# Performance work log

Hardware: AMD Instinct MI355X
Metric: run time of the kernel (lower is better)

Reference implementation:

```python
import jax, jax.numpy as jnp
import numpy as np

N = 50000      # total nodes
E = 800000     # total edges (before self-loops)
B = 512        # graphs in batch
H = 4          # attention heads
D = 64         # per-head dim (hidden 256 = H*D)
F_IN = 203     # node feature dim
HID = H * D
NEG_SLOPE = 0.2  # PyG GATConv LeakyReLU default
LN_EPS = 1e-5


def setup_inputs() -> dict:
    key = jax.random.key(0)
    ks = jax.random.split(key, 24)
    g = lambda k, shape, fan: (jax.random.normal(k, shape, jnp.float32) / np.sqrt(fan))
    inp = {
        "x": jax.random.normal(ks[0], (N, F_IN), jnp.float32),
        "edge_index": jax.random.randint(ks[1], (2, E), 0, N, jnp.int64),
        "edge_weight": jax.random.uniform(ks[2], (E,), jnp.float32),
        "batch": jnp.sort(jax.random.randint(ks[3], (N,), 0, B, jnp.int64)),
        # GAT layer 1 params
        "W1": g(ks[4], (HID, F_IN), F_IN),
        "a_s1": g(ks[5], (H, D), D),
        "a_d1": g(ks[6], (H, D), D),
        "a_e1": g(ks[7], (H, D), D),
        "We1": g(ks[8], (HID, 1), 1),
        "b1": jnp.zeros((HID,), jnp.float32),
        # GAT layer 2 params
        "W2": g(ks[9], (HID, HID), HID),
        "a_s2": g(ks[10], (H, D), D),
        "a_d2": g(ks[11], (H, D), D),
        "a_e2": g(ks[12], (H, D), D),
        "We2": g(ks[13], (HID, 1), 1),
        "b2": jnp.zeros((HID,), jnp.float32),
        # LayerNorms
        "ln1_g": jnp.ones((HID,), jnp.float32),
        "ln1_b": jnp.zeros((HID,), jnp.float32),
        "ln2_g": jnp.ones((HID,), jnp.float32),
        "ln2_b": jnp.zeros((HID,), jnp.float32),
    }
    return inp


def _gat(x, src, dst, e_attr, W, a_s, a_d, a_e, We, bias, n_nodes):
    # projected node features: [N, H, D]
    xp = (x @ W.T).reshape(n_nodes, H, D)
    alpha_src = jnp.einsum('nhd,hd->nh', xp, a_s)   # [N, H]
    alpha_dst = jnp.einsum('nhd,hd->nh', xp, a_d)   # [N, H]
    ep = (e_attr @ We.T).reshape(-1, H, D)          # [E', H, D]
    alpha_edge = jnp.einsum('ehd,hd->eh', ep, a_e)  # [E', H]
    logits = jax.nn.leaky_relu(alpha_src[src] + alpha_dst[dst] + alpha_edge, NEG_SLOPE)
    # segment softmax over incoming edges per destination node
    m = jax.ops.segment_max(logits, dst, num_segments=n_nodes)
    ex = jnp.exp(logits - m[dst])
    denom = jax.ops.segment_sum(ex, dst, num_segments=n_nodes)
    alpha = ex / denom[dst]                          # [E', H]
    msg = alpha[:, :, None] * xp[src]                # [E', H, D]
    out = jax.ops.segment_sum(msg, dst, num_segments=n_nodes)
    return out.reshape(n_nodes, HID) + bias


def _ln(x, g, b):
    mu = x.mean(-1, keepdims=True)
    var = ((x - mu) ** 2).mean(-1, keepdims=True)
    return (x - mu) * jax.lax.rsqrt(var + LN_EPS) * g + b


def reference(x, edge_index, edge_weight, batch,
              W1, a_s1, a_d1, a_e1, We1, b1,
              W2, a_s2, a_d2, a_e2, We2, b2,
              ln1_g, ln1_b, ln2_g, ln2_b):
    n = x.shape[0]
    # PyG GATConv add_self_loops=True, edge_attr fill_value='mean'
    loop = jnp.arange(n)
    src = jnp.concatenate([edge_index[0], loop])
    dst = jnp.concatenate([edge_index[1], loop])
    ew = jnp.concatenate([edge_weight, jnp.full((n,), edge_weight.mean(), edge_weight.dtype)])
    e_attr = ew[:, None]  # edge_dim = 1

    h = _gat(x, src, dst, e_attr, W1, a_s1, a_d1, a_e1, We1, b1, n)
    h = jax.nn.elu(_ln(h, ln1_g, ln1_b))  # dropout omitted (eval mode)
    h = _gat(h, src, dst, e_attr, W2, a_s2, a_d2, a_e2, We2, b2, n)
    h = jax.nn.elu(_ln(h, ln2_g, ln2_b))

    # global_mean_pool
    s = jax.ops.segment_sum(h, batch, num_segments=B)
    cnt = jax.ops.segment_sum(jnp.ones((n,), h.dtype), batch, num_segments=B)
    return s / jnp.maximum(cnt, 1.0)[:, None]
```

## Files before the change

### kernel.cpp

```cpp
#include <hip/hip_runtime.h>
#include <math.h>

#define HID 256
#define NEG_SLOPE 0.2f
#define LN_EPS 1e-5f

typedef __attribute__((ext_vector_type(4))) float f32x4;
typedef __attribute__((ext_vector_type(8))) short bf16x8;
typedef __attribute__((address_space(3))) unsigned char lds_b;
typedef const __attribute__((address_space(1))) unsigned char glob_b;

__device__ __forceinline__ float bf2f_lo(unsigned int u) {
    union { unsigned int i; float f; } c; c.i = u << 16; return c.f;
}
__device__ __forceinline__ float bf2f_hi(unsigned int u) {
    union { unsigned int i; float f; } c; c.i = u & 0xffff0000u; return c.f;
}
__device__ __forceinline__ float bf2f_u(unsigned short u) {
    union { unsigned int i; float f; } c; c.i = ((unsigned int)u) << 16; return c.f;
}
__device__ __forceinline__ unsigned short f2bf(float f) {
    union { float f; unsigned int i; } c; c.f = f;
    unsigned int i = c.i;
    return (unsigned short)((i + 0x7fffu + ((i >> 16) & 1u)) >> 16);
}

__global__ __launch_bounds__(256) void k_pre(const float* __restrict__ ew, int E,
                                             const int* __restrict__ ei, int N, int EN, int NH,
                                             float* __restrict__ partials, int* __restrict__ deg,
                                             const float* __restrict__ W1, const float* __restrict__ W2,
                                             unsigned short* __restrict__ o1, unsigned short* __restrict__ o2, int K1,
                                             const float* __restrict__ x, unsigned short* __restrict__ x16, int FIN) {
    int t = threadIdx.x;
    int b = blockIdx.x;
    if (b < 256) {
        __shared__ float sdata[4];
        float v = 0.f;
        for (int i = b * 256 + t; i < E; i += 65536) v += ew[i];
        for (int o = 32; o; o >>= 1) v += __shfl_xor(v, o);
        if ((t & 63) == 0) sdata[t >> 6] = v;
        __syncthreads();
        if (t == 0) partials[b] = sdata[0] + sdata[1] + sdata[2] + sdata[3];
    } else if (b < 256 + NH) {
        int i = (b - 256) * 1024 + t;
        int e0 = i, e1 = i + 256, e2 = i + 512, e3 = i + 768;
        bool v0 = e0 < EN, v1 = e1 < EN, v2 = e2 < EN, v3 = e3 < EN;
        int d0 = v0 ? ((e0 < E) ? ei[E + e0] : e0 - E) : 0;
        int d1 = v1 ? ((e1 < E) ? ei[E + e1] : e1 - E) : 0;
        int d2 = v2 ? ((e2 < E) ? ei[E + e2] : e2 - E) : 0;
        int d3 = v3 ? ((e3 < E) ? ei[E + e3] : e3 - E) : 0;
        if (v0) atomicAdd(&deg[d0], 1);
        if (v1) atomicAdd(&deg[d1], 1);
        if (v2) atomicAdd(&deg[d2], 1);
        if (v3) atomicAdd(&deg[d3], 1);
    } else if (b < 256 + NH + 512) {
        int wb = b - 256 - NH;
        const float* in = (wb < 256) ? W1 : W2;
        unsigned short* out = (wb < 256) ? o1 : o2;
        int K = (wb < 256) ? K1 : 256;
        int col = wb & 255;
        float v = (t < K) ? in[(size_t)col * K + t] : 0.f;
        int ks = t >> 5, j = (t >> 3) & 3, e = t & 7;
        out[ks * 8192 + j * 2048 + ((((col << 4) ^ (j << 4))) >> 1) + e] = f2bf(v);
    } else {
        int r = b - 256 - NH - 512;
        x16[(size_t)r * 256 + t] = (t < FIN) ? f2bf(x[(size_t)r * FIN + t]) : (unsigned short)0;
    }
}

__global__ __launch_bounds__(256) void k_scanred_coeff(const int* __restrict__ deg, int N, int NB,
                                                       int* __restrict__ bsum,
                                                       const float* __restrict__ partials, float* __restrict__ sumw,
                                                       const float* __restrict__ We1, const float* __restrict__ ae1,
                                                       const float* __restrict__ We2, const float* __restrict__ ae2,
                                                       float* __restrict__ c1, float* __restrict__ c2) {
    int t = threadIdx.x;
    int b = blockIdx.x;
    if (b < NB) {
        __shared__ int sdata[4];
        int i = b * 256 + t;
        int v = (i < N) ? deg[i] : 0;
        for (int o = 32; o; o >>= 1) v += __shfl_xor(v, o);
        if ((t & 63) == 0) sdata[t >> 6] = v;
        __syncthreads();
        if (t == 0) bsum[b] = sdata[0] + sdata[1] + sdata[2] + sdata[3];
    } else if (b == NB) {
        __shared__ float sdata[4];
        float v = partials[t];
        for (int o = 32; o; o >>= 1) v += __shfl_xor(v, o);
        if ((t & 63) == 0) sdata[t >> 6] = v;
        __syncthreads();
        if (t == 0) *sumw = sdata[0] + sdata[1] + sdata[2] + sdata[3];
    } else {
        float v1 = We1[t] * ae1[t];
        float v2 = We2[t] * ae2[t];
        for (int o = 1; o < 64; o <<= 1) { v1 += __shfl_xor(v1, o); v2 += __shfl_xor(v2, o); }
        if ((t & 63) == 0) { c1[t >> 6] = v1; c2[t >> 6] = v2; }
    }
}

__global__ __launch_bounds__(256) void k_scan_apply(const int* __restrict__ deg, int N, int NB,
                                                    const int* __restrict__ bsum,
                                                    int* __restrict__ offs, int* __restrict__ cursor) {
    __shared__ int sm[256];
    __shared__ int sb[256];
    int t = threadIdx.x;
    int i = blockIdx.x * 256 + t;
    int v = (i < N) ? deg[i] : 0;
    int vb = (t < NB) ? bsum[t] : 0;
    sm[t] = v;
    sb[t] = vb;
    __syncthreads();
    for (int o = 1; o < 256; o <<= 1) {
        int tv = (t >= o) ? sm[t - o] : 0;
        int tb = (t >= o) ? sb[t - o] : 0;
        __syncthreads();
        sm[t] += tv;
        sb[t] += tb;
        __syncthreads();
    }
    int myb = bsum[blockIdx.x];
    int boff = sb[blockIdx.x] - myb;
    if (i < N) {
        int e = boff + sm[t] - v;
        offs[i] = e; cursor[i] = e;
        if (i == N - 1) offs[N] = boff + sm[t];
    }
}

__global__ __launch_bounds__(256) void k_scatter(const int* __restrict__ ei, int E, int EN,
                                                 int* __restrict__ cursor, int* __restrict__ csr_eid) {
    int i = blockIdx.x * 1024 + threadIdx.x;
    int e0 = i, e1 = i + 256, e2 = i + 512, e3 = i + 768;
    bool v0 = e0 < EN, v1 = e1 < EN, v2 = e2 < EN, v3 = e3 < EN;
    int d0 = v0 ? ((e0 < E) ? ei[E + e0] : e0 - E) : 0;
    int d1 = v1 ? ((e1 < E) ? ei[E + e1] : e1 - E) : 0;
    int d2 = v2 ? ((e2 < E) ? ei[E + e2] : e2 - E) : 0;
    int d3 = v3 ? ((e3 < E) ? ei[E + e3] : e3 - E) : 0;
    int p0 = v0 ? atomicAdd(&cursor[d0], 1) : 0;
    int p1 = v1 ? atomicAdd(&cursor[d1], 1) : 0;
    int p2 = v2 ? atomicAdd(&cursor[d2], 1) : 0;
    int p3 = v3 ? atomicAdd(&cursor[d3], 1) : 0;
    if (v0) csr_eid[p0] = e0;
    if (v1) csr_eid[p1] = e1;
    if (v2) csr_eid[p2] = e2;
    if (v3) csr_eid[p3] = e3;
}

__device__ __forceinline__ void gemm_dev(int bid,
    const unsigned short* __restrict__ A16, const unsigned short* __restrict__ Bt16, int M,
    const float* __restrict__ asf, const float* __restrict__ adf,
    unsigned short* __restrict__ C16, float* __restrict__ as_out, float* __restrict__ ad_out)
{
    __shared__ __align__(16) unsigned short Bsl[4 * 256 * 8];
    int t = threadIdx.x;
    int lane = t & 63, w = t >> 6;
    int row0 = bid << 5;
    int kg = lane >> 4, fr = lane & 15;

    int ar0 = row0 + fr;      if (ar0 >= M) ar0 = 0;
    int ar1 = row0 + 16 + fr; if (ar1 >= M) ar1 = 0;
    const unsigned short* ap0 = A16 + (size_t)ar0 * 256 + (kg << 3);
    const unsigned short* ap1 = A16 + (size_t)ar1 * 256 + (kg << 3);

    f32x4 acc[2][4];
#pragma unroll
    for (int i = 0; i < 2; i++)
#pragma unroll
        for (int j = 0; j < 4; j++) acc[i][j] = (f32x4){0.f, 0.f, 0.f, 0.f};

    for (int ks = 0; ks < 8; ks++) {
#pragma unroll
        for (int j = 0; j < 4; j++) {
            __builtin_amdgcn_global_load_lds(
                (glob_b*)(Bt16 + (size_t)ks * 8192 + j * 2048 + t * 8),
                (lds_b*)((char*)Bsl + j * 4096 + t * 16),
                16, 0, 0);
        }
        bf16x8 a0 = *(const bf16x8*)(ap0 + (ks << 5));
        bf16x8 a1 = *(const bf16x8*)(ap1 + (ks << 5));
        __syncthreads();
#pragma unroll
        for (int nf = 0; nf < 4; nf++) {
            int col = (w << 6) + (nf << 4) + fr;
            bf16x8 bv = *(const bf16x8*)((const char*)Bsl + (kg << 12) + (((col << 4)) ^ (kg << 4)));
            acc[0][nf] = __builtin_amdgcn_mfma_f32_16x16x32_bf16(a0, bv, acc[0][nf], 0, 0, 0);
            acc[1][nf] = __builtin_amdgcn_mfma_f32_16x16x32_bf16(a1, bv, acc[1][nf], 0, 0, 0);
        }
        __syncthreads();
    }

#pragma unroll
    for (int mf = 0; mf < 2; mf++)
#pragma unroll
        for (int j = 0; j < 4; j++) {
            int gr = row0 + mf * 16 + kg * 4 + j;
            if (gr < M) {
#pragma unroll
                for (int nf = 0; nf < 4; nf++)
                    C16[(size_t)gr * 256 + (w << 6) + (nf << 4) + fr] = f2bf(acc[mf][nf][j]);
            }
        }
    float asv[4], adv[4];
#pragma unroll
    for (int nf = 0; nf < 4; nf++) {
        int col = (w << 6) + (nf << 4) + fr;
        asv[nf] = asf[col]; adv[nf] = adf[col];
    }
#pragma unroll
    for (int mf = 0; mf < 2; mf++)
#pragma unroll
        for (int j = 0; j < 4; j++) {
            float ps = acc[mf][0][j] * asv[0] + acc[mf][1][j] * asv[1] + acc[mf][2][j] * asv[2] + acc[mf][3][j] * asv[3];
            float pd = acc[mf][0][j] * adv[0] + acc[mf][1][j] * adv[1] + acc[mf][2][j] * adv[2] + acc[mf][3][j] * adv[3];
#pragma unroll
            for (int o = 1; o < 16; o <<= 1) { ps += __shfl_xor(ps, o); pd += __shfl_xor(pd, o); }
            if (fr == 0) {
                int gr = row0 + mf * 16 + kg * 4 + j;
                if (gr < M) {
                    as_out[gr * 4 + w] = ps;
                    ad_out[gr * 4 + w] = pd;
                }
            }
        }
}

__device__ __forceinline__ void sort_gather_dev(int bid, const int* __restrict__ offs, int* __restrict__ eid,
                                                const int* __restrict__ ei, const float* __restrict__ ew,
                                                const float* __restrict__ sumw, int E, int N,
                                                int* __restrict__ csr_src, float* __restrict__ csr_w) {
    int lane = threadIdx.x & 63;
    int n = (bid << 2) + (threadIdx.x >> 6);
    if (n >= N) return;
    int s0 = offs[n];
    int d = offs[n + 1] - s0;
    if (d <= 0) return;
    if (d <= 64) {
        int key = (lane < d) ? eid[s0 + lane] : 0x7fffffff;
        int rank = 0;
        for (int j = 0; j < d; j++) {
            int kj = __shfl(key, j);
            rank += (kj < key) ? 1 : 0;
        }
        if (lane < d) {
            int s; float wv;
            if (key < E) { s = ei[key]; wv = ew[key]; }
            else         { s = key - E; wv = *sumw / (float)E; }
            csr_src[s0 + rank] = s;
            csr_w[s0 + rank] = wv;
        }
    } else {
        if (lane == 0) {
            for (int i = s0 + 1; i < s0 + d; i++) {
                int ke = eid[i];
                int j = i - 1;
                while (j >= s0 && eid[j] > ke) { eid[j + 1] = eid[j]; j--; }
                eid[j + 1] = ke;
            }
        }
        __builtin_amdgcn_wave_barrier();
        for (int i = lane; i < d; i += 64) {
            int e = eid[s0 + i];
            int s; float wv;
            if (e < E) { s = ei[e]; wv = ew[e]; }
            else       { s = e - E; wv = *sumw / (float)E; }
            csr_src[s0 + i] = s;
            csr_w[s0 + i] = wv;
        }
    }
}

__global__ __launch_bounds__(256) void k_gemm_sort(int MB,
    const unsigned short* __restrict__ A16, const unsigned short* __restrict__ Bt16, int M,
    const float* __restrict__ asf, const float* __restrict__ adf,
    unsigned short* __restrict__ C16, float* __restrict__ as_out, float* __restrict__ ad_out,
    const int* __restrict__ offs, int* __restrict__ eid,
    const int* __restrict__ ei, const float* __restrict__ ew,
    const float* __restrict__ sumw, int E,
    int* __restrict__ csr_src, float* __restrict__ csr_w) {
    if ((int)blockIdx.x < MB)
        gemm_dev(blockIdx.x, A16, Bt16, M, asf, adf, C16, as_out, ad_out);
    else
        sort_gather_dev(blockIdx.x - MB, offs, eid, ei, ew, sumw, E, M, csr_src, csr_w);
}

__global__ __launch_bounds__(256) void gemm_mfma(
    const unsigned short* __restrict__ A16, const unsigned short* __restrict__ Bt16, int M,
    const float* __restrict__ asf, const float* __restrict__ adf,
    unsigned short* __restrict__ C16, float* __restrict__ as_out, float* __restrict__ ad_out) {
    gemm_dev(blockIdx.x, A16, Bt16, M, asf, adf, C16, as_out, ad_out);
}

#define ACC8(u, q) do { \
    acc0 += (q) * bf2f_lo((u).x); acc1 += (q) * bf2f_hi((u).x); \
    acc2 += (q) * bf2f_lo((u).y); acc3 += (q) * bf2f_hi((u).y); \
    acc4 += (q) * bf2f_lo((u).z); acc5 += (q) * bf2f_hi((u).z); \
    acc6 += (q) * bf2f_lo((u).w); acc7 += (q) * bf2f_hi((u).w); } while (0)

__global__ __launch_bounds__(256) void gat_kernel(
    const unsigned short* __restrict__ xp16, const int* __restrict__ offs,
    const int* __restrict__ csr_src, const float* __restrict__ csr_w,
    const float* __restrict__ as_, const float* __restrict__ ad_,
    const float* __restrict__ cvec, const float* __restrict__ bias,
    const float* __restrict__ ln_g, const float* __restrict__ ln_b,
    int N, unsigned short* __restrict__ out16) {
    __shared__ float p_lds[4][256];
    __shared__ int   s_lds[4][64];
    int lane = threadIdx.x & 63;
    int wid = threadIdx.x >> 6;
    int n = (blockIdx.x << 2) + wid;
    if (n >= N) return;
    int start = offs[n], end = offs[n + 1];
    int e0 = lane >> 5;
    int colb = lane & 31;
    int hq2 = colb >> 3;
    const unsigned short* xbase = xp16 + (size_t)colb * 8;
    float4 adv = *(const float4*)(ad_ + (size_t)n * 4);
    float c0 = cvec[0], c1 = cvec[1], c2 = cvec[2], c3 = cvec[3];
    float m = -INFINITY, dn = 0.f;
    float acc0 = 0, acc1 = 0, acc2 = 0, acc3 = 0, acc4 = 0, acc5 = 0, acc6 = 0, acc7 = 0;

    for (int base = start; base < end; base += 64) {
        int idx = base + lane;
        bool act = idx < end;
        int s = act ? csr_src[idx] : 0;
        float w = act ? csr_w[idx] : 0.f;
        float4 av = *(const float4*)(as_ + (size_t)s * 4);
        float l0 = av.x + adv.x + w * c0; l0 = l0 >= 0.f ? l0 : NEG_SLOPE * l0;
        float l1 = av.y + adv.y + w * c1; l1 = l1 >= 0.f ? l1 : NEG_SLOPE * l1;
        float l2 = av.z + adv.z + w * c2; l2 = l2 >= 0.f ? l2 : NEG_SLOPE * l2;
        float l3 = av.w + adv.w + w * c3; l3 = l3 >= 0.f ? l3 : NEG_SLOPE * l3;
        float lm = fmaxf(fmaxf(l0, l1), fmaxf(l2, l3));
        if (!act) lm = -INFINITY;
        for (int o = 32; o; o >>= 1) lm = fmaxf(lm, __shfl_xor(lm, o));
        float nm = fmaxf(m, lm);
        float sc = __expf(m - nm);
        m = nm;
        dn *= sc;
        acc0 *= sc; acc1 *= sc; acc2 *= sc; acc3 *= sc;
        acc4 *= sc; acc5 *= sc; acc6 *= sc; acc7 *= sc;
        float p0 = act ? __expf(l0 - m) : 0.f;
        float p1 = act ? __expf(l1 - m) : 0.f;
        float p2 = act ? __expf(l2 - m) : 0.f;
        float p3 = act ? __expf(l3 - m) : 0.f;
        float4 pv = { p0, p1, p2, p3 };
        *(float4*)&p_lds[wid][lane << 2] = pv;
        s_lds[wid][lane] = s;
        int cnt = end - base; if (cnt > 64) cnt = 64;
        int k = 0;
        for (; k + 8 <= cnt; k += 8) {
            int i0 = k + e0, i1 = k + 2 + e0, i2 = k + 4 + e0, i3 = k + 6 + e0;
            int s0 = s_lds[wid][i0], s1 = s_lds[wid][i1], s2 = s_lds[wid][i2], s3 = s_lds[wid][i3];
            uint4 u0 = *(const uint4*)(xbase + (size_t)s0 * 256);
            uint4 u1 = *(const uint4*)(xbase + (size_t)s1 * 256);
            uint4 u2 = *(const uint4*)(xbase + (size_t)s2 * 256);
            uint4 u3 = *(const uint4*)(xbase + (size_t)s3 * 256);
            float q0 = p_lds[wid][(i0 << 2) + hq2];
            float q1 = p_lds[wid][(i1 << 2) + hq2];
            float q2 = p_lds[wid][(i2 << 2) + hq2];
            float q3 = p_lds[wid][(i3 << 2) + hq2];
            dn += q0 + q1 + q2 + q3;
            ACC8(u0, q0); ACC8(u1, q1); ACC8(u2, q2); ACC8(u3, q3);
        }
        for (; k < cnt; k += 2) {
            int i = k + e0;
            bool v = i < cnt;
            int si = s_lds[wid][v ? i : 0];
            float qi = v ? p_lds[wid][(i << 2) + hq2] : 0.f;
            uint4 u = *(const uint4*)(xbase + (size_t)si * 256);
            dn += qi;
            ACC8(u, qi);
        }
    }
    acc0 += __shfl_xor(acc0, 32); acc1 += __shfl_xor(acc1, 32);
    acc2 += __shfl_xor(acc2, 32); acc3 += __shfl_xor(acc3, 32);
    acc4 += __shfl_xor(acc4, 32); acc5 += __shfl_xor(acc5, 32);
    acc6 += __shfl_xor(acc6, 32); acc7 += __shfl_xor(acc7, 32);
    dn += __shfl_xor(dn, 32);
    float inv = 1.f / dn;
    int cb8 = colb << 3;
    float4 bA = *(const float4*)(bias + cb8);
    float4 bB = *(const float4*)(bias + cb8 + 4);
    float o0 = acc0 * inv + bA.x, o1 = acc1 * inv + bA.y, o2 = acc2 * inv + bA.z, o3 = acc3 * inv + bA.w;
    float o4 = acc4 * inv + bB.x, o5 = acc5 * inv + bB.y, o6 = acc6 * inv + bB.z, o7 = acc7 * inv + bB.w;
    float part = ((o0 + o1) + (o2 + o3)) + ((o4 + o5) + (o6 + o7));
    for (int o = 16; o; o >>= 1) part += __shfl_xor(part, o);
    float mu = part * (1.f / 256.f);
    float d0 = o0 - mu, d1 = o1 - mu, d2 = o2 - mu, d3 = o3 - mu;
    float d4 = o4 - mu, d5 = o5 - mu, d6 = o6 - mu, d7 = o7 - mu;
    float vpart = ((d0 * d0 + d1 * d1) + (d2 * d2 + d3 * d3)) + ((d4 * d4 + d5 * d5) + (d6 * d6 + d7 * d7));
    for (int o = 16; o; o >>= 1) vpart += __shfl_xor(vpart, o);
    float rstd = rsqrtf(vpart * (1.f / 256.f) + LN_EPS);
    float4 gA = *(const float4*)(ln_g + cb8), gB = *(const float4*)(ln_g + cb8 + 4);
    float4 eA = *(const float4*)(ln_b + cb8), eB = *(const float4*)(ln_b + cb8 + 4);
    float y0 = d0 * rstd * gA.x + eA.x; y0 = y0 > 0.f ? y0 : __expf(y0) - 1.f;
    float y1 = d1 * rstd * gA.y + eA.y; y1 = y1 > 0.f ? y1 : __expf(y1) - 1.f;
    float y2 = d2 * rstd * gA.z + eA.z; y2 = y2 > 0.f ? y2 : __expf(y2) - 1.f;
    float y3 = d3 * rstd * gA.w + eA.w; y3 = y3 > 0.f ? y3 : __expf(y3) - 1.f;
    float y4 = d4 * rstd * gB.x + eB.x; y4 = y4 > 0.f ? y4 : __expf(y4) - 1.f;
    float y5 = d5 * rstd * gB.y + eB.y; y5 = y5 > 0.f ? y5 : __expf(y5) - 1.f;
    float y6 = d6 * rstd * gB.z + eB.z; y6 = y6 > 0.f ? y6 : __expf(y6) - 1.f;
    float y7 = d7 * rstd * gB.w + eB.w; y7 = y7 > 0.f ? y7 : __expf(y7) - 1.f;
    if (lane < 32) {
        uint4 ov;
        ov.x = ((unsigned int)f2bf(y1) << 16) | f2bf(y0);
        ov.y = ((unsigned int)f2bf(y3) << 16) | f2bf(y2);
        ov.z = ((unsigned int)f2bf(y5) << 16) | f2bf(y4);
        ov.w = ((unsigned int)f2bf(y7) << 16) | f2bf(y6);
        *(uint4*)(out16 + (size_t)n * HID + cb8) = ov;
    }
}

__device__ __forceinline__ int lower_bound_i(const int* a, int n, int key) {
    int lo = 0, hi = n;
    while (lo < hi) { int mid = (lo + hi) >> 1; if (a[mid] < key) lo = mid + 1; else hi = mid; }
    return lo;
}

__global__ __launch_bounds__(256) void pool_kernel(const unsigned short* __restrict__ h, const int* __restrict__ batch,
                                                   int N, float* __restrict__ out) {
    int b = blockIdx.x;
    int lo = lower_bound_i(batch, N, b);
    int hi = lower_bound_i(batch, N, b + 1);
    float a0 = 0.f, a1 = 0.f, a2 = 0.f, a3 = 0.f;
    int n = lo;
    for (; n + 4 <= hi; n += 4) {
        a0 += bf2f_u(h[(size_t)(n + 0) * HID + threadIdx.x]);
        a1 += bf2f_u(h[(size_t)(n + 1) * HID + threadIdx.x]);
        a2 += bf2f_u(h[(size_t)(n + 2) * HID + threadIdx.x]);
        a3 += bf2f_u(h[(size_t)(n + 3) * HID + threadIdx.x]);
    }
    for (; n < hi; n++) a0 += bf2f_u(h[(size_t)n * HID + threadIdx.x]);
    float acc = (a0 + a1) + (a2 + a3);
    out[(size_t)b * HID + threadIdx.x] = acc / fmaxf((float)(hi - lo), 1.f);
}

extern "C" void kernel_launch(void* const* d_in, const int* in_sizes, int n_in,
                              void* d_out, int out_size, void* d_ws, size_t ws_size,
                              hipStream_t stream) {
    const float* x    = (const float*)d_in[0];
    const int*   ei   = (const int*)d_in[1];
    const float* ew   = (const float*)d_in[2];
    const int*   batch= (const int*)d_in[3];
    const float* W1   = (const float*)d_in[4];
    const float* as1  = (const float*)d_in[5];
    const float* ad1  = (const float*)d_in[6];
    const float* ae1  = (const float*)d_in[7];
    const float* We1  = (const float*)d_in[8];
    const float* b1   = (const float*)d_in[9];
    const float* W2   = (const float*)d_in[10];
    const float* as2  = (const float*)d_in[11];
    const float* ad2  = (const float*)d_in[12];
    const float* ae2  = (const float*)d_in[13];
    const float* We2  = (const float*)d_in[14];
    const float* b2   = (const float*)d_in[15];
    const float* ln1g = (const float*)d_in[16];
    const float* ln1b = (const float*)d_in[17];
    const float* ln2g = (const float*)d_in[18];
    const float* ln2b = (const float*)d_in[19];

    int N = in_sizes[3];
    int E = in_sizes[2];
    int FIN = in_sizes[0] / N;
    int EN = E + N;
    int B = out_size / HID;
    float* outp = (float*)d_out;
    int NB = (N + 255) / 256;
    int NH = (EN + 1023) / 1024;

    char* ws = (char*)d_ws;
    size_t off = 0;
    auto alloc = [&](size_t bytes) { void* p = ws + off; off = (off + bytes + 255) & ~(size_t)255; return p; };
    float* sumw    = (float*)alloc(4);
    int*   deg     = (int*)  alloc((size_t)N * 4);
    size_t zero_bytes = 256 + (size_t)N * 4;
    float* partials= (float*)alloc(256 * 4);
    int*   bsum    = (int*)  alloc(256 * 4);
    int*   offs    = (int*)  alloc((size_t)(N + 1) * 4);
    int*   cursor  = (int*)  alloc((size_t)N * 4);
    int*   csr_eid = (int*)  alloc((size_t)EN * 4);
    int*   csr_src = (int*)  alloc((size_t)EN * 4);
    float* csr_w   = (float*)alloc((size_t)EN * 4);
    float* asb     = (float*)alloc((size_t)N * 4 * 4);
    float* adb     = (float*)alloc((size_t)N * 4 * 4);
    float* cc      = (float*)alloc(64);
    unsigned short* w1_16 = (unsigned short*)alloc((size_t)HID * HID * 2);
    unsigned short* w2_16 = (unsigned short*)alloc((size_t)HID * HID * 2);
    unsigned short* x16   = (unsigned short*)alloc((size_t)N * HID * 2);
    unsigned short* xp16  = (unsigned short*)alloc((size_t)N * HID * 2);
    (void)ws_size; (void)n_in;

    int MB = (N + 31) / 32;

    (void)hipMemsetAsync(d_ws, 0, zero_bytes, stream);
    k_pre<<<256 + NH + 512 + N, 256, 0, stream>>>(ew, E, ei, N, EN, NH, partials, deg,
                                                  W1, W2, w1_16, w2_16, FIN, x, x16, FIN);
    k_scanred_coeff<<<NB + 2, 256, 0, stream>>>(deg, N, NB, bsum, partials, sumw, We1, ae1, We2, ae2, cc, cc + 4);
    k_scan_apply<<<NB, 256, 0, stream>>>(deg, N, NB, bsum, offs, cursor);
    k_scatter<<<(EN + 1023) / 1024, 256, 0, stream>>>(ei, E, EN, cursor, csr_eid);
    k_gemm_sort<<<MB + (N + 3) / 4, 256, 0, stream>>>(MB, x16, w1_16, N, as1, ad1, xp16, asb, adb,
                                                      offs, csr_eid, ei, ew, sumw, E, csr_src, csr_w);
    gat_kernel<<<(N + 3) / 4, 256, 0, stream>>>(xp16, offs, csr_src, csr_w, asb, adb, cc, b1, ln1g, ln1b, N, x16);
    gemm_mfma<<<MB, 256, 0, stream>>>(x16, w2_16, N, as2, ad2, xp16, asb, adb);
    gat_kernel<<<(N + 3) / 4, 256, 0, stream>>>(xp16, offs, csr_src, csr_w, asb, adb, cc + 4, b2, ln2g, ln2b, N, x16);
    pool_kernel<<<B, 256, 0, stream>>>(x16, batch, N, outp);
}
```

Baseline: 351.0 us.

## Fuse edge scatter with layer-1 GEMM and fold CSR sort into first GAT

```diff
diff --git a/kernel.cpp b/kernel.cpp
--- a/kernel.cpp
+++ b/kernel.cpp
@@ -128,25 +128,6 @@
     }
 }
 
-__global__ __launch_bounds__(256) void k_scatter(const int* __restrict__ ei, int E, int EN,
-                                                 int* __restrict__ cursor, int* __restrict__ csr_eid) {
-    int i = blockIdx.x * 1024 + threadIdx.x;
-    int e0 = i, e1 = i + 256, e2 = i + 512, e3 = i + 768;
-    bool v0 = e0 < EN, v1 = e1 < EN, v2 = e2 < EN, v3 = e3 < EN;
-    int d0 = v0 ? ((e0 < E) ? ei[E + e0] : e0 - E) : 0;
-    int d1 = v1 ? ((e1 < E) ? ei[E + e1] : e1 - E) : 0;
-    int d2 = v2 ? ((e2 < E) ? ei[E + e2] : e2 - E) : 0;
-    int d3 = v3 ? ((e3 < E) ? ei[E + e3] : e3 - E) : 0;
-    int p0 = v0 ? atomicAdd(&cursor[d0], 1) : 0;
-    int p1 = v1 ? atomicAdd(&cursor[d1], 1) : 0;
-    int p2 = v2 ? atomicAdd(&cursor[d2], 1) : 0;
-    int p3 = v3 ? atomicAdd(&cursor[d3], 1) : 0;
-    if (v0) csr_eid[p0] = e0;
-    if (v1) csr_eid[p1] = e1;
-    if (v2) csr_eid[p2] = e2;
-    if (v3) csr_eid[p3] = e3;
-}
-
 __device__ __forceinline__ void gemm_dev(int bid,
     const unsigned short* __restrict__ A16, const unsigned short* __restrict__ Bt16, int M,
     const float* __restrict__ asf, const float* __restrict__ adf,
@@ -225,63 +206,33 @@
         }
 }
 
-__device__ __forceinline__ void sort_gather_dev(int bid, const int* __restrict__ offs, int* __restrict__ eid,
-                                                const int* __restrict__ ei, const float* __restrict__ ew,
-                                                const float* __restrict__ sumw, int E, int N,
-                                                int* __restrict__ csr_src, float* __restrict__ csr_w) {
-    int lane = threadIdx.x & 63;
-    int n = (bid << 2) + (threadIdx.x >> 6);
-    if (n >= N) return;
-    int s0 = offs[n];
-    int d = offs[n + 1] - s0;
-    if (d <= 0) return;
-    if (d <= 64) {
-        int key = (lane < d) ? eid[s0 + lane] : 0x7fffffff;
-        int rank = 0;
-        for (int j = 0; j < d; j++) {
-            int kj = __shfl(key, j);
-            rank += (kj < key) ? 1 : 0;
-        }
-        if (lane < d) {
-            int s; float wv;
-            if (key < E) { s = ei[key]; wv = ew[key]; }
-            else         { s = key - E; wv = *sumw / (float)E; }
-            csr_src[s0 + rank] = s;
-            csr_w[s0 + rank] = wv;
-        }
+__global__ __launch_bounds__(256) void k_scatter_gemm(int NSc, const int* __restrict__ ei, int E, int EN,
+                                                      int* __restrict__ cursor, int* __restrict__ csr_eid,
+                                                      const unsigned short* __restrict__ A16,
+                                                      const unsigned short* __restrict__ Bt16, int M,
+                                                      const float* __restrict__ asf, const float* __restrict__ adf,
+                                                      unsigned short* __restrict__ C16,
+                                                      float* __restrict__ as_out, float* __restrict__ ad_out) {
+    int b = blockIdx.x;
+    if (b < NSc) {
+        int i = b * 1024 + threadIdx.x;
+        int e0 = i, e1 = i + 256, e2 = i + 512, e3 = i + 768;
+        bool v0 = e0 < EN, v1 = e1 < EN, v2 = e2 < EN, v3 = e3 < EN;
+        int d0 = v0 ? ((e0 < E) ? ei[E + e0] : e0 - E) : 0;
+        int d1 = v1 ? ((e1 < E) ? ei[E + e1] : e1 - E) : 0;
+        int d2 = v2 ? ((e2 < E) ? ei[E + e2] : e2 - E) : 0;
+        int d3 = v3 ? ((e3 < E) ? ei[E + e3] : e3 - E) : 0;
+        int p0 = v0 ? atomicAdd(&cursor[d0], 1) : 0;
+        int p1 = v1 ? atomicAdd(&cursor[d1], 1) : 0;
+        int p2 = v2 ? atomicAdd(&cursor[d2], 1) : 0;
+        int p3 = v3 ? atomicAdd(&cursor[d3], 1) : 0;
+        if (v0) csr_eid[p0] = e0;
+        if (v1) csr_eid[p1] = e1;
+        if (v2) csr_eid[p2] = e2;
+        if (v3) csr_eid[p3] = e3;
     } else {
-        if (lane == 0) {
-            for (int i = s0 + 1; i < s0 + d; i++) {
-                int ke = eid[i];
-                int j = i - 1;
-                while (j >= s0 && eid[j] > ke) { eid[j + 1] = eid[j]; j--; }
-                eid[j + 1] = ke;
-            }
-        }
-        __builtin_amdgcn_wave_barrier();
-        for (int i = lane; i < d; i += 64) {
-            int e = eid[s0 + i];
-            int s; float wv;
-            if (e < E) { s = ei[e]; wv = ew[e]; }
-            else       { s = e - E; wv = *sumw / (float)E; }
-            csr_src[s0 + i] = s;
-            csr_w[s0 + i] = wv;
-        }
-    }
-}
-
-__global__ __launch_bounds__(256) void k_gemm_sort(int MB,
-    const unsigned short* __restrict__ A16, const unsigned short* __restrict__ Bt16, int M,
-    const float* __restrict__ asf, const float* __restrict__ adf,
-    unsigned short* __restrict__ C16, float* __restrict__ as_out, float* __restrict__ ad_out,
-    const int* __restrict__ offs, int* __restrict__ eid,
-    const int* __restrict__ ei, const float* __restrict__ ew,
-    const float* __restrict__ sumw, int E,
-    int* __restrict__ csr_src, float* __restrict__ csr_w) {
-    if ((int)blockIdx.x < MB)
-        gemm_dev(blockIdx.x, A16, Bt16, M, asf, adf, C16, as_out, ad_out);
-    else
-        sort_gather_dev(blockIdx.x - MB, offs, eid, ei, ew, sumw, E, M, csr_src, csr_w);
+        gemm_dev(b - NSc, A16, Bt16, M, asf, adf, C16, as_out, ad_out);
+    }
 }
 
 __global__ __launch_bounds__(256) void gemm_mfma(
@@ -297,9 +248,12 @@
     acc4 += (q) * bf2f_lo((u).z); acc5 += (q) * bf2f_hi((u).z); \
     acc6 += (q) * bf2f_lo((u).w); acc7 += (q) * bf2f_hi((u).w); } while (0)
 
+template<int BUILD>
 __global__ __launch_bounds__(256) void gat_kernel(
     const unsigned short* __restrict__ xp16, const int* __restrict__ offs,
-    const int* __restrict__ csr_src, const float* __restrict__ csr_w,
+    int* __restrict__ csr_eid, const int* __restrict__ ei, const float* __restrict__ ew,
+    const float* __restrict__ sumw, int E,
+    int* __restrict__ csr_src, float* __restrict__ csr_w,
     const float* __restrict__ as_, const float* __restrict__ ad_,
     const float* __restrict__ cvec, const float* __restrict__ bias,
     const float* __restrict__ ln_g, const float* __restrict__ ln_b,
@@ -311,6 +265,22 @@
     int n = (blockIdx.x << 2) + wid;
     if (n >= N) return;
     int start = offs[n], end = offs[n + 1];
+    int dtot = end - start;
+    float wfill = 0.f;
+    if (BUILD) {
+        wfill = *sumw / (float)E;
+        if (dtot > 64) {
+            if (lane == 0) {
+                for (int i = start + 1; i < end; i++) {
+                    int ke = csr_eid[i];
+                    int j = i - 1;
+                    while (j >= start && csr_eid[j] > ke) { csr_eid[j + 1] = csr_eid[j]; j--; }
+                    csr_eid[j + 1] = ke;
+                }
+            }
+            __threadfence();
+        }
+    }
     int e0 = lane >> 5;
     int colb = lane & 31;
     int hq2 = colb >> 3;
@@ -323,8 +293,28 @@
     for (int base = start; base < end; base += 64) {
         int idx = base + lane;
         bool act = idx < end;
-        int s = act ? csr_src[idx] : 0;
-        float w = act ? csr_w[idx] : 0.f;
+        int cnt = end - base; if (cnt > 64) cnt = 64;
+        int s; float w;
+        if (BUILD) {
+            int key = act ? csr_eid[idx] : 0x7fffffff;
+            if (dtot <= 64) {
+                int rank = 0;
+                for (int j = 0; j < cnt; j++) {
+                    int kj = __shfl(key, j);
+                    rank += (kj < key) ? 1 : 0;
+                }
+                key = __builtin_amdgcn_ds_permute(rank << 2, key);
+            }
+            if (act) {
+                if (key < E) { s = ei[key]; w = ew[key]; }
+                else         { s = key - E; w = wfill; }
+                csr_src[idx] = s;
+                csr_w[idx] = w;
+            } else { s = 0; w = 0.f; }
+        } else {
+            s = act ? csr_src[idx] : 0;
+            w = act ? csr_w[idx] : 0.f;
+        }
         float4 av = *(const float4*)(as_ + (size_t)s * 4);
         float l0 = av.x + adv.x + w * c0; l0 = l0 >= 0.f ? l0 : NEG_SLOPE * l0;
         float l1 = av.y + adv.y + w * c1; l1 = l1 >= 0.f ? l1 : NEG_SLOPE * l1;
@@ -346,7 +336,6 @@
         float4 pv = { p0, p1, p2, p3 };
         *(float4*)&p_lds[wid][lane << 2] = pv;
         s_lds[wid][lane] = s;
-        int cnt = end - base; if (cnt > 64) cnt = 64;
         int k = 0;
         for (; k + 8 <= cnt; k += 8) {
             int i0 = k + e0, i1 = k + 2 + e0, i2 = k + 4 + e0, i3 = k + 6 + e0;
@@ -467,6 +456,7 @@
     float* outp = (float*)d_out;
     int NB = (N + 255) / 256;
     int NH = (EN + 1023) / 1024;
+    int NSc = (EN + 1023) / 1024;
 
     char* ws = (char*)d_ws;
     size_t off = 0;
@@ -497,11 +487,12 @@
                                                   W1, W2, w1_16, w2_16, FIN, x, x16, FIN);
     k_scanred_coeff<<<NB + 2, 256, 0, stream>>>(deg, N, NB, bsum, partials, sumw, We1, ae1, We2, ae2, cc, cc + 4);
     k_scan_apply<<<NB, 256, 0, stream>>>(deg, N, NB, bsum, offs, cursor);
-    k_scatter<<<(EN + 1023) / 1024, 256, 0, stream>>>(ei, E, EN, cursor, csr_eid);
-    k_gemm_sort<<<MB + (N + 3) / 4, 256, 0, stream>>>(MB, x16, w1_16, N, as1, ad1, xp16, asb, adb,
-                                                      offs, csr_eid, ei, ew, sumw, E, csr_src, csr_w);
-    gat_kernel<<<(N + 3) / 4, 256, 0, stream>>>(xp16, offs, csr_src, csr_w, asb, adb, cc, b1, ln1g, ln1b, N, x16);
+    k_scatter_gemm<<<NSc + MB, 256, 0, stream>>>(NSc, ei, E, EN, cursor, csr_eid,
+                                                 x16, w1_16, N, as1, ad1, xp16, asb, adb);
+    gat_kernel<1><<<(N + 3) / 4, 256, 0, stream>>>(xp16, offs, csr_eid, ei, ew, sumw, E, csr_src, csr_w,
+                                                   asb, adb, cc, b1, ln1g, ln1b, N, x16);
     gemm_mfma<<<MB, 256, 0, stream>>>(x16, w2_16, N, as2, ad2, xp16, asb, adb);
-    gat_kernel<<<(N + 3) / 4, 256, 0, stream>>>(xp16, offs, csr_src, csr_w, asb, adb, cc + 4, b2, ln2g, ln2b, N, x16);
+    gat_kernel<0><<<(N + 3) / 4, 256, 0, stream>>>(xp16, offs, csr_eid, ei, ew, sumw, E, csr_src, csr_w,
+                                                   asb, adb, cc + 4, b2, ln2g, ln2b, N, x16);
     pool_kernel<<<B, 256, 0, stream>>>(x16, batch, N, outp);
 }
```

After: 357.6 us. Within noise of the previous version (+1.9%).
